# Optimization experiments

Hardware: AMD Instinct MI355X
Metric: run time of the kernel (lower is better)

## Reference

```python
import jax, jax.numpy as jnp
import numpy as np

K = 3
THRESHOLD = 0.05
RADIUS = 0.1
MIN_CORR = 3
MAX_CORR = 1500
N_ITER = 5
EPS = 1e-5
P, N = 1024, 128


def setup_inputs() -> dict:
    key = jax.random.key(0)
    k1, k2, k3, k4, k5 = jax.random.split(key, 5)
    # local knn patches: small spatial extent so matching_radius=0.1 is meaningful
    ref_knn_points = jax.random.normal(k1, (P, N, 3), jnp.float32) * 0.05
    src_knn_points = jax.random.normal(k2, (P, N, 3), jnp.float32) * 0.05
    ref_knn_masks = jax.random.uniform(k3, (P, N)) > 0.1
    src_knn_masks = jax.random.uniform(k4, (P, N)) > 0.1
    matching_score_map = jax.random.normal(k5, (P, N, N), jnp.float32)
    return {
        'ref_knn_points': ref_knn_points,
        'src_knn_points': src_knn_points,
        'ref_knn_masks': ref_knn_masks,
        'src_knn_masks': src_knn_masks,
        'matching_score_map': matching_score_map,
    }


def _kabsch(H, src_c, ref_c, bad):
    # guard degenerate (all-zero-weight) problems with a fixed full-rank H
    safe = jnp.diag(jnp.asarray([3.0, 2.0, 1.0], H.dtype))
    H = jnp.where(bad[..., None, None], safe, H)
    U, S, Vt = jnp.linalg.svd(H)
    V = jnp.swapaxes(Vt, -1, -2)
    Ut = jnp.swapaxes(U, -1, -2)
    det = jnp.linalg.det(V @ Ut)
    D = jnp.zeros_like(H).at[..., 0, 0].set(1.0).at[..., 1, 1].set(1.0).at[..., 2, 2].set(det)
    R = V @ D @ Ut
    t = ref_c - jnp.einsum('...cd,...d->...c', R, src_c)
    T = jnp.zeros(H.shape[:-2] + (4, 4), H.dtype)
    return T.at[..., :3, :3].set(R).at[..., :3, 3].set(t).at[..., 3, 3].set(1.0)


def pair_procrustes(src, ref, w):
    # src, ref: (..., M, 3); w: (..., M)
    tot = jnp.sum(w, -1, keepdims=True)
    wn = w / (tot + EPS)
    src_c = jnp.einsum('...m,...mc->...c', wn, src)
    ref_c = jnp.einsum('...m,...mc->...c', wn, ref)
    H = jnp.einsum('...mc,...m,...md->...cd', src - src_c[..., None, :], wn, ref - ref_c[..., None, :])
    return _kabsch(H, src_c, ref_c, tot[..., 0] < EPS)


def grid_procrustes(src, ref, W):
    # per-proposal weighted Procrustes over the full (ref_i, src_j) pair grid;
    # identical math to gathering nonzero pairs since zero-weight pairs drop out
    tot = jnp.sum(W, (1, 2))  # (P,)
    Wn = W / (tot[:, None, None] + EPS)
    ref_c = jnp.einsum('pij,pic->pc', Wn, ref)
    src_c = jnp.einsum('pij,pjc->pc', Wn, src)
    H = jnp.einsum('pjc,pij,pid->pcd', src - src_c[:, None], Wn, ref - ref_c[:, None])
    return _kabsch(H, src_c, ref_c, tot < EPS)


def _forward(ref_knn_points, src_knn_points, ref_knn_masks, src_knn_masks, matching_score_map):
    Pn, Nn, _ = matching_score_map.shape
    sm = jnp.exp(matching_score_map)
    corr_mask = ref_knn_masks[:, :, None] & src_knn_masks[:, None, :]

    pidx = jnp.arange(Pn)[:, None, None]
    lidx = jnp.arange(Nn)[None, :, None]
    # topk over src dim -> ref_score_map
    ref_ts, ref_ti = jax.lax.top_k(sm, K)
    ref_score_map = jnp.zeros_like(sm).at[pidx, lidx, ref_ti].set(ref_ts)
    # topk over ref dim -> src_score_map (via transpose)
    smT = jnp.swapaxes(sm, 1, 2)
    src_ts, src_ti = jax.lax.top_k(smT, K)
    src_score_map = jnp.swapaxes(jnp.zeros_like(smT).at[pidx, lidx, src_ti].set(src_ts), 1, 2)

    ref_corr = (ref_score_map > THRESHOLD) & corr_mask
    src_corr = (src_score_map > THRESHOLD) & corr_mask
    score_map = 0.5 * (ref_score_map + src_score_map)
    corr_map = ref_corr & src_corr

    # per-proposal Procrustes with pair-grid weights (zero weight = not a corr)
    W = jnp.where(corr_map, score_map, 0.0)
    counts = jnp.sum(corr_map, (1, 2))
    valid = counts >= MIN_CORR
    transforms = grid_procrustes(src_knn_points, ref_knn_points, W)  # (P,4,4)

    # global capped correspondence pool (top MAX_CORR by score)
    flat = jnp.where(corr_map, score_map, -1.0).reshape(-1)
    top_scores, top_flat = jax.lax.top_k(flat, MAX_CORR)
    p = top_flat // (Nn * Nn)
    rem = top_flat % (Nn * Nn)
    i = rem // Nn
    j = rem % Nn
    real = top_scores > 0.0  # padded slots if fewer than MAX_CORR corrs
    corr_scores = jnp.where(real, top_scores, 0.0)
    ref_pts = ref_knn_points[p, i]   # (M,3)
    src_pts = src_knn_points[p, j]   # (M,3)
    # padded candidates pushed far away so they are never inliers
    src_eval = src_pts + jnp.where(real, 0.0, 1e6)[:, None]

    # evaluate every proposal transform on the capped pool, pick max-inlier
    aligned = jnp.einsum('pcd,md->pmc', transforms[:, :3, :3], src_eval) + transforms[:, None, :3, 3]
    d2 = jnp.sum((ref_pts[None] - aligned) ** 2, -1)  # (P,M)
    inliers = d2 < RADIUS ** 2
    icount = jnp.where(valid, jnp.sum(inliers, 1), -1)
    best = jnp.argmax(icount)

    cur = corr_scores * inliers[best].astype(corr_scores.dtype)
    T = pair_procrustes(src_pts, ref_pts, cur)
    for _ in range(N_ITER - 1):
        al = src_eval @ T[:3, :3].T + T[:3, 3]
        d2 = jnp.sum((ref_pts - al) ** 2, -1)
        cur = corr_scores * (d2 < RADIUS ** 2).astype(corr_scores.dtype)
        T = pair_procrustes(src_pts, ref_pts, cur)

    return ref_pts, src_pts, corr_scores, T


def reference(ref_knn_points, src_knn_points, ref_knn_masks, src_knn_masks, matching_score_map):
    return _forward(ref_knn_points, src_knn_points, ref_knn_masks, src_knn_masks, matching_score_map)
```

## Files before the change

kernel.cpp:

```cpp
#include <hip/hip_runtime.h>
#include <math.h>

#define PP    1024
#define NPT   128
#define NN2   16384
#define THRESH 0.05f
#define MAXC  1500
#define EPSD  1e-5
#define RRD   (0.1*0.1)
#define NEGF  -3.0e38f
#define MAXCPB 384
#define SELCAP 4096u

#define OFF_CCNT  0
#define OFF_ICNT  4096
#define OFF_TRANS 8192
#define OFF_POOL  106496
#define OFF_HDR   166496
#define OFF_SEL   166560
#define OFF_PHIST 199328
#define OFF_CLIST 1247904

__device__ inline void top3_upd(float v, float& a, float& b, float& c) {
  float m1 = fminf(a, v);
  a = fmaxf(a, v);
  float m2 = fminf(b, m1);
  b = fmaxf(b, m1);
  c = fmaxf(c, m2);
}
__device__ inline void merge3(float& a, float& b, float& c, float x0, float x1, float x2) {
  float z0 = fmaxf(a, x0);
  float z1 = fmaxf(fminf(a, x0), fmaxf(b, x1));
  float z2 = fmaxf(fmaxf(c, x2), fmaxf(fminf(b, x0), fminf(a, x1)));
  a = z0; b = z1; c = z2;
}

__device__ inline unsigned enc_f(float v) {
  unsigned b = __float_as_uint(v);
  return (b & 0x80000000u) ? ~b : (b | 0x80000000u);
}
__device__ inline float dec_f(unsigned enc) {
  unsigned b = (enc & 0x80000000u) ? (enc ^ 0x80000000u) : ~enc;
  return __uint_as_float(b);
}

__device__ inline void jacobi4(double A[4][4], double V[4][4]) {
  for (int i = 0; i < 4; ++i)
    for (int j = 0; j < 4; ++j) V[i][j] = (i == j) ? 1.0 : 0.0;
  const int PI_[6] = {0, 0, 0, 1, 1, 2};
  const int QI_[6] = {1, 2, 3, 2, 3, 3};
  for (int sweep = 0; sweep < 30; ++sweep) {
    double off = fabs(A[0][1]) + fabs(A[0][2]) + fabs(A[0][3]) +
                 fabs(A[1][2]) + fabs(A[1][3]) + fabs(A[2][3]);
    double dia = fabs(A[0][0]) + fabs(A[1][1]) + fabs(A[2][2]) + fabs(A[3][3]);
    if (off <= 1e-14 * (dia + 1e-300)) break;
    for (int r = 0; r < 6; ++r) {
      int p = PI_[r], q = QI_[r];
      double apq = A[p][q];
      if (fabs(apq) <= 1e-18 * (fabs(A[p][p]) + fabs(A[q][q]) + 1e-300)) continue;
      double theta = (A[q][q] - A[p][p]) / (2.0 * apq);
      double t = ((theta >= 0.0) ? 1.0 : -1.0) / (fabs(theta) + sqrt(1.0 + theta * theta));
      double c = 1.0 / sqrt(1.0 + t * t);
      double s = t * c;
      for (int k = 0; k < 4; ++k) {
        double akp = A[k][p], akq = A[k][q];
        A[k][p] = c * akp - s * akq;
        A[k][q] = s * akp + c * akq;
      }
      for (int k = 0; k < 4; ++k) {
        double apk = A[p][k], aqk = A[q][k];
        A[p][k] = c * apk - s * aqk;
        A[q][k] = s * apk + c * aqk;
      }
      for (int k = 0; k < 4; ++k) {
        double vkp = V[k][p], vkq = V[k][q];
        V[k][p] = c * vkp - s * vkq;
        V[k][q] = s * vkp + c * vkq;
      }
    }
  }
}

__device__ inline double cof3(const double M[4][4], int rr, int cc) {
  int ri[3], ci[3];
  int n = 0;
  for (int i = 0; i < 4; ++i) if (i != rr) ri[n++] = i;
  n = 0;
  for (int j = 0; j < 4; ++j) if (j != cc) ci[n++] = j;
  double a = M[ri[0]][ci[0]], b = M[ri[0]][ci[1]], c = M[ri[0]][ci[2]];
  double d = M[ri[1]][ci[0]], e = M[ri[1]][ci[1]], f = M[ri[1]][ci[2]];
  double g = M[ri[2]][ci[0]], h = M[ri[2]][ci[1]], i2 = M[ri[2]][ci[2]];
  double m = a * (e * i2 - f * h) - b * (d * i2 - f * g) + c * (d * h - e * g);
  return (((rr + cc) & 1) ? -m : m);
}

__device__ inline void kabsch_from_sums(double tot, const double* sr, const double* ss,
                                        const double* m9, double* T12) {
  double den = tot + EPSD;
  double rc[3], sc[3];
  for (int c = 0; c < 3; ++c) { rc[c] = sr[c] / den; sc[c] = ss[c] / den; }
  double sb = tot / den;
  double H[3][3];
  for (int c = 0; c < 3; ++c)
    for (int d = 0; d < 3; ++d)
      H[c][d] = m9[c * 3 + d] / den - (2.0 - sb) * sc[c] * rc[d];
  if (tot < EPSD) {
    H[0][0] = 3.0; H[0][1] = 0.0; H[0][2] = 0.0;
    H[1][0] = 0.0; H[1][1] = 2.0; H[1][2] = 0.0;
    H[2][0] = 0.0; H[2][1] = 0.0; H[2][2] = 1.0;
  }
  double Sxx = H[0][0], Sxy = H[0][1], Sxz = H[0][2];
  double Syx = H[1][0], Syy = H[1][1], Syz = H[1][2];
  double Szx = H[2][0], Szy = H[2][1], Szz = H[2][2];
  double N[4][4] = {
    {Sxx + Syy + Szz, Syz - Szy,        Szx - Sxz,         Sxy - Syx},
    {Syz - Szy,       Sxx - Syy - Szz,  Sxy + Syx,         Szx + Sxz},
    {Szx - Sxz,       Sxy + Syx,       -Sxx + Syy - Szz,   Syz + Szy},
    {Sxy - Syx,       Szx + Sxz,        Syz + Szy,        -Sxx - Syy + Szz}};
  double fro2 = Sxx*Sxx + Sxy*Sxy + Sxz*Sxz + Syx*Syx + Syy*Syy + Syz*Syz +
                Szx*Szx + Szy*Szy + Szz*Szz;
  double c2 = -2.0 * fro2;
  double c1 = -8.0 * (Sxx * (Syy * Szz - Syz * Szy) -
                      Sxy * (Syx * Szz - Syz * Szx) +
                      Sxz * (Syx * Szy - Syy * Szx));
  double c0 = N[0][0] * cof3(N, 0, 0) + N[0][1] * cof3(N, 0, 1) +
              N[0][2] * cof3(N, 0, 2) + N[0][3] * cof3(N, 0, 3);
  double lam = -1e300;
  for (int i = 0; i < 4; ++i) {
    double r = N[i][i];
    for (int j = 0; j < 4; ++j) if (j != i) r += fabs(N[i][j]);
    lam = fmax(lam, r);
  }
  for (int it = 0; it < 100; ++it) {
    double l2 = lam * lam;
    double pv = ((l2 + c2) * lam + c1) * lam + c0;
    double dp = (4.0 * l2 + 2.0 * c2) * lam + c1;
    if (dp == 0.0) break;
    double d = pv / dp;
    lam -= d;
    if (fabs(d) <= 1e-14 * fmax(fabs(lam), 1e-30)) break;
  }
  double K[4][4];
  for (int i = 0; i < 4; ++i)
    for (int j = 0; j < 4; ++j) K[i][j] = N[i][j];
  for (int i = 0; i < 4; ++i) K[i][i] -= lam;
  int jb = 0;
  double bestd = -1.0;
  for (int j = 0; j < 4; ++j) {
    double dj = fabs(cof3(K, j, j));
    if (dj > bestd) { bestd = dj; jb = j; }
  }
  double v[4];
  for (int i = 0; i < 4; ++i) v[i] = cof3(K, jb, i);
  double vn2 = v[0]*v[0] + v[1]*v[1] + v[2]*v[2] + v[3]*v[3];
  double scl = sqrt(fro2) + fabs(lam) + 1e-300;
  double thr = 1e-10 * scl * scl * scl;
  double q0, qx, qy, qz;
  if (vn2 > thr * thr) {
    double inv = 1.0 / sqrt(vn2);
    q0 = v[0] * inv; qx = v[1] * inv; qy = v[2] * inv; qz = v[3] * inv;
  } else {
    double A[4][4], V[4][4];
    for (int i = 0; i < 4; ++i)
      for (int j = 0; j < 4; ++j) A[i][j] = N[i][j];
    jacobi4(A, V);
    int kb = 0; double ev = A[0][0];
    for (int i = 1; i < 4; ++i) if (A[i][i] > ev) { ev = A[i][i]; kb = i; }
    double w0 = V[0][kb], w1 = V[1][kb], w2 = V[2][kb], w3 = V[3][kb];
    double nr = sqrt(w0*w0 + w1*w1 + w2*w2 + w3*w3);
    if (nr < 1e-300) { w0 = 1.0; w1 = w2 = w3 = 0.0; nr = 1.0; }
    q0 = w0 / nr; qx = w1 / nr; qy = w2 / nr; qz = w3 / nr;
  }
  double R[3][3];
  R[0][0] = q0*q0 + qx*qx - qy*qy - qz*qz; R[0][1] = 2.0*(qx*qy - q0*qz); R[0][2] = 2.0*(qx*qz + q0*qy);
  R[1][0] = 2.0*(qx*qy + q0*qz); R[1][1] = q0*q0 - qx*qx + qy*qy - qz*qz; R[1][2] = 2.0*(qy*qz - q0*qx);
  R[2][0] = 2.0*(qx*qz - q0*qy); R[2][1] = 2.0*(qy*qz + q0*qx); R[2][2] = q0*q0 - qx*qx - qy*qy + qz*qz;
  for (int c = 0; c < 3; ++c)
    for (int d = 0; d < 3; ++d) T12[c * 3 + d] = R[c][d];
  for (int c = 0; c < 3; ++c)
    T12[9 + c] = rc[c] - (R[c][0] * sc[0] + R[c][1] * sc[1] + R[c][2] * sc[2]);
}

__global__ __launch_bounds__(256, 2) void k_fused(
    const float* __restrict__ scores, const void* __restrict__ mref,
    const void* __restrict__ msrc, unsigned* __restrict__ ccnt,
    unsigned long long* __restrict__ clist) {
  const int p = blockIdx.x;
  const int tid = threadIdx.x;
  __shared__ float tile[128 * 132];
  __shared__ float colpart[2][NPT][3];
  __shared__ float rthr[NPT], cthr[NPT];
  __shared__ unsigned char lmr[NPT];
  __shared__ unsigned lcnt;
  __shared__ unsigned masku8_s;
  if (tid == 0) lcnt = 0;
  if (tid < 64) {
    unsigned v = (tid < 32) ? ((const unsigned*)mref)[p * 32 + tid]
                            : ((const unsigned*)msrc)[p * 32 + (tid - 32)];
    unsigned long long any = __ballot(v > 1u);
    if (tid == 0) masku8_s = any ? 1u : 0u;
  }
  {
    const float4* S4 = (const float4*)(scores + (size_t)p * NN2);
    float4 vv[16];
#pragma unroll
    for (int s = 0; s < 16; ++s)
      vv[s] = S4[s * 256 + tid];
#pragma unroll
    for (int s = 0; s < 16; ++s) {
      int flat = (s * 256 + tid) * 4;
      int r = flat >> 7, c = flat & 127;
      *(float4*)&tile[r * 132 + c] = vv[s];
    }
  }
  __syncthreads();
  const unsigned maskU8 = masku8_s;
  if (tid < NPT)
    lmr[tid] = maskU8 ? (((const unsigned char*)mref)[p * NPT + tid] != 0)
                      : (((const int*)mref)[p * NPT + tid] != 0);
  const int col = tid & 127;
  const int half = tid >> 7;
  const bool msj = maskU8 ? (((const unsigned char*)msrc)[p * NPT + col] != 0)
                          : (((const int*)msrc)[p * NPT + col] != 0);
  for (int rb = 0; rb < 4; ++rb) {
    int r = rb * 32 + (tid >> 3);
    int o = tid & 7;
    float a = NEGF, b = NEGF, c = NEGF;
    const float4* tr = (const float4*)&tile[r * 132 + o * 16];
#pragma unroll
    for (int k = 0; k < 4; ++k) {
      float4 q = tr[k];
      top3_upd(q.x, a, b, c); top3_upd(q.y, a, b, c);
      top3_upd(q.z, a, b, c); top3_upd(q.w, a, b, c);
    }
#pragma unroll
    for (int m = 1; m < 8; m <<= 1) {
      float pa = __shfl_xor(a, m, 64), pb = __shfl_xor(b, m, 64), pc = __shfl_xor(c, m, 64);
      merge3(a, b, c, pa, pb, pc);
    }
    if (o == 0) rthr[r] = c;
  }
  {
    float a = NEGF, b = NEGF, c = NEGF;
    const float* tc = tile + (half * 64) * 132 + col;
#pragma unroll 8
    for (int r = 0; r < 64; ++r)
      top3_upd(tc[r * 132], a, b, c);
    colpart[half][col][0] = a; colpart[half][col][1] = b; colpart[half][col][2] = c;
  }
  __syncthreads();
  if (tid < NPT) {
    float a = colpart[0][tid][0], b = colpart[0][tid][1], c = colpart[0][tid][2];
    merge3(a, b, c, colpart[1][tid][0], colpart[1][tid][1], colpart[1][tid][2]);
    cthr[tid] = c;
  }
  __syncthreads();
  {
    const float cth = cthr[col];
    const float* tc = tile + (half * 64) * 132 + col;
#pragma unroll 4
    for (int it = 0; it < 64; ++it) {
      float v = tc[it * 132];
      int i = half * 64 + it;
      if (msj && v >= cth && v >= rthr[i] && lmr[i] && (expf(v) > THRESH)) {
        unsigned pos = atomicAdd(&lcnt, 1u);
        if (pos < MAXCPB) {
          unsigned long long key =
              (((unsigned long long)(~enc_f(v))) << 32) |
              (unsigned long long)(unsigned)(p * NN2 + i * NPT + col);
          clist[(size_t)p * MAXCPB + pos] = key;
        }
      }
    }
  }
  __syncthreads();
  if (tid == 0) ccnt[p] = (lcnt < MAXCPB) ? lcnt : MAXCPB;
}

__global__ __launch_bounds__(256) void k_hist(
    const unsigned* __restrict__ ccnt, const unsigned long long* __restrict__ clist,
    unsigned* __restrict__ phist) {
  __shared__ unsigned lh[4096];
  const int b = blockIdx.x, tid = threadIdx.x;
  for (int i = tid; i < 4096; i += 256) lh[i] = 0;
  __syncthreads();
  for (int q = 0; q < 16; ++q) {
    const int p = b * 16 + q;
    const unsigned cnt = min(ccnt[p], (unsigned)MAXCPB);
    const unsigned long long* my = clist + (size_t)p * MAXCPB;
    for (unsigned t = tid; t < cnt; t += 256)
      atomicAdd(&lh[(unsigned)(my[t] >> 52)], 1u);
  }
  __syncthreads();
  for (int i = tid; i < 4096; i += 256) phist[b * 4096 + i] = lh[i];
}

__global__ __launch_bounds__(1024) void k_cut(const unsigned* __restrict__ phist,
                                              unsigned* __restrict__ hdr) {
  __shared__ unsigned s[1024];
  __shared__ unsigned cb_s;
  const int tid = threadIdx.x;
  if (tid == 0) cb_s = 4095u;
  uint4 acc = make_uint4(0, 0, 0, 0);
  const uint4* ph4 = (const uint4*)phist;
#pragma unroll 4
  for (int b = 0; b < 64; ++b) {
    uint4 h = ph4[b * 1024 + tid];
    acc.x += h.x; acc.y += h.y; acc.z += h.z; acc.w += h.w;
  }
  s[tid] = acc.x + acc.y + acc.z + acc.w;
  __syncthreads();
  for (int off = 1; off < 1024; off <<= 1) {
    unsigned v = s[tid];
    unsigned a = (tid >= off) ? s[tid - off] : 0u;
    __syncthreads();
    s[tid] = v + a;
    __syncthreads();
  }
  {
    unsigned pre = (tid > 0) ? s[tid - 1] : 0u;
    unsigned tot4 = acc.x + acc.y + acc.z + acc.w;
    if (pre < MAXC && pre + tot4 >= MAXC) {
      unsigned c0 = pre + acc.x, c1 = c0 + acc.y, c2 = c1 + acc.z;
      cb_s = (c0 >= MAXC) ? tid * 4 : (c1 >= MAXC) ? tid * 4 + 1
           : (c2 >= MAXC) ? tid * 4 + 2 : tid * 4 + 3;
    }
  }
  __syncthreads();
  if (tid == 0) {
    hdr[0] = s[1023];
    hdr[1] = 0u;
    hdr[2] = cb_s;
  }
}

__global__ __launch_bounds__(256) void k_gather(
    const unsigned* __restrict__ ccnt, const unsigned long long* __restrict__ clist,
    unsigned* __restrict__ hdr, unsigned long long* __restrict__ sel) {
  const int b = blockIdx.x, tid = threadIdx.x, lane = tid & 63;
  const unsigned cut = hdr[2];
  for (int q = 0; q < 16; ++q) {
    const int p = b * 16 + q;
    const unsigned cnt = min(ccnt[p], (unsigned)MAXCPB);
    const unsigned long long* my = clist + (size_t)p * MAXCPB;
    for (unsigned t0 = 0; t0 < cnt; t0 += 256) {
      unsigned t = t0 + tid;
      unsigned long long key = 0;
      bool take = false;
      if (t < cnt) {
        key = my[t];
        take = ((unsigned)(key >> 52)) <= cut;
      }
      unsigned long long mb = __ballot(take);
      if (mb) {
        int leader = __ffsll((unsigned long long)mb) - 1;
        unsigned base = 0;
        if (lane == leader) base = atomicAdd(&hdr[1], (unsigned)__popcll(mb));
        base = __shfl(base, leader, 64);
        if (take) {
          unsigned pos = base + (unsigned)__popcll(mb & ((1ull << lane) - 1ull));
          if (pos < SELCAP) sel[pos] = key;
        }
      }
    }
  }
}

__global__ __launch_bounds__(1024) void k_sortout(
    const unsigned long long* __restrict__ sel, const unsigned* __restrict__ hdr,
    const float* __restrict__ refp, const float* __restrict__ srcp,
    float* __restrict__ pool, float* __restrict__ out) {
  __shared__ unsigned long long keys[4096];
  const int tid = threadIdx.x;
  const unsigned sc = min(hdr[1], SELCAP);
  for (unsigned t = tid; t < 4096u; t += 1024)
    keys[t] = (t < sc) ? sel[t] : 0xFFFFFFFFFFFFFFFFull;
  __syncthreads();
  for (unsigned k = 2; k <= 4096; k <<= 1) {
    for (unsigned j = k >> 1; j; j >>= 1) {
      for (unsigned t = tid; t < 4096; t += 1024) {
        unsigned ixj = t ^ j;
        if (ixj > t) {
          unsigned long long A = keys[t], B = keys[ixj];
          bool up = ((t & k) == 0);
          if (up ? (A > B) : (A < B)) { keys[t] = B; keys[ixj] = A; }
        }
      }
      __syncthreads();
    }
  }
  const unsigned stotal = hdr[0];
  const unsigned nreal = (stotal < MAXC) ? stotal : MAXC;
  for (int mm = tid; mm < MAXC; mm += 1024) {
    unsigned flat; float score; bool real = ((unsigned)mm < nreal);
    if (real) {
      unsigned long long key = keys[mm];
      flat = (unsigned)(key & 0xFFFFFFFFull);
      score = expf(dec_f(~(unsigned)(key >> 32)));
    } else {
      flat = (unsigned)mm;
      score = 0.f;
    }
    unsigned p = flat >> 14, rem = flat & 16383u, i = rem >> 7, j = rem & 127u;
    float rx = refp[((size_t)p * NPT + i) * 3 + 0];
    float ry = refp[((size_t)p * NPT + i) * 3 + 1];
    float rz = refp[((size_t)p * NPT + i) * 3 + 2];
    float sx = srcp[((size_t)p * NPT + j) * 3 + 0];
    float sy = srcp[((size_t)p * NPT + j) * 3 + 1];
    float sz = srcp[((size_t)p * NPT + j) * 3 + 2];
    out[mm * 3 + 0] = rx; out[mm * 3 + 1] = ry; out[mm * 3 + 2] = rz;
    out[4500 + mm * 3 + 0] = sx; out[4500 + mm * 3 + 1] = sy; out[4500 + mm * 3 + 2] = sz;
    out[9000 + mm] = score;
    pool[mm * 3 + 0] = rx; pool[mm * 3 + 1] = ry; pool[mm * 3 + 2] = rz;
    pool[4500 + mm * 3 + 0] = sx; pool[4500 + mm * 3 + 1] = sy; pool[4500 + mm * 3 + 2] = sz;
    float pad = real ? 0.f : 1e6f;
    pool[9000 + mm * 3 + 0] = sx + pad;
    pool[9000 + mm * 3 + 1] = sy + pad;
    pool[9000 + mm * 3 + 2] = sz + pad;
    pool[13500 + mm] = score;
  }
}

__global__ __launch_bounds__(256) void k_evalT(
    const unsigned* __restrict__ ccnt, const unsigned long long* __restrict__ clist,
    const float* __restrict__ refp, const float* __restrict__ srcp,
    const float* __restrict__ pool, double* __restrict__ trans,
    int* __restrict__ icount) {
  const int p = blockIdx.x, tid = threadIdx.x, lane = tid & 63;
  __shared__ double red[4][16];
  __shared__ double Ts[12];
  __shared__ int redc[4];
  const unsigned cnt = min(ccnt[p], (unsigned)MAXCPB);
  double tot = 0, sr0 = 0, sr1 = 0, sr2 = 0, ss0 = 0, ss1 = 0, ss2 = 0;
  double m00 = 0, m01 = 0, m02 = 0, m10 = 0, m11 = 0, m12 = 0, m20 = 0, m21 = 0, m22 = 0;
  for (unsigned t = tid; t < cnt; t += 256) {
    unsigned long long key = clist[(size_t)p * MAXCPB + t];
    unsigned flat = (unsigned)(key & 0xFFFFFFFFull);
    unsigned rem = flat & 16383u, i = rem >> 7, j = rem & 127u;
    double w = (double)expf(dec_f(~(unsigned)(key >> 32)));
    double rx = refp[((size_t)p * NPT + i) * 3 + 0];
    double ry = refp[((size_t)p * NPT + i) * 3 + 1];
    double rz = refp[((size_t)p * NPT + i) * 3 + 2];
    double sx = srcp[((size_t)p * NPT + j) * 3 + 0];
    double sy = srcp[((size_t)p * NPT + j) * 3 + 1];
    double sz = srcp[((size_t)p * NPT + j) * 3 + 2];
    tot += w;
    sr0 += w * rx; sr1 += w * ry; sr2 += w * rz;
    ss0 += w * sx; ss1 += w * sy; ss2 += w * sz;
    double wsx = w * sx, wsy = w * sy, wsz = w * sz;
    m00 += wsx * rx; m01 += wsx * ry; m02 += wsx * rz;
    m10 += wsy * rx; m11 += wsy * ry; m12 += wsy * rz;
    m20 += wsz * rx; m21 += wsz * ry; m22 += wsz * rz;
  }
  double vals[16] = {tot, sr0, sr1, sr2, ss0, ss1, ss2,
                     m00, m01, m02, m10, m11, m12, m20, m21, m22};
#pragma unroll
  for (int k = 0; k < 16; ++k) {
    double x = vals[k];
    for (int o = 32; o; o >>= 1) x += __shfl_down(x, o, 64);
    if (lane == 0) red[tid >> 6][k] = x;
  }
  __syncthreads();
  if (tid == 0) {
    double s16[16];
    for (int k = 0; k < 16; ++k)
      s16[k] = red[0][k] + red[1][k] + red[2][k] + red[3][k];
    kabsch_from_sums(s16[0], s16 + 1, s16 + 4, s16 + 7, Ts);
    for (int k = 0; k < 12; ++k) trans[p * 12 + k] = Ts[k];
  }
  __syncthreads();
  double R00 = Ts[0], R01 = Ts[1], R02 = Ts[2], R10 = Ts[3], R11 = Ts[4], R12 = Ts[5];
  double R20 = Ts[6], R21 = Ts[7], R22 = Ts[8], t0 = Ts[9], t1 = Ts[10], t2 = Ts[11];
  const float* pr = pool;
  const float* pe = pool + 9000;
  int c = 0;
  for (int mm = tid; mm < MAXC; mm += 256) {
    double ex = pe[mm * 3], ey = pe[mm * 3 + 1], ez = pe[mm * 3 + 2];
    double ax = R00 * ex + R01 * ey + R02 * ez + t0;
    double ay = R10 * ex + R11 * ey + R12 * ez + t1;
    double az = R20 * ex + R21 * ey + R22 * ez + t2;
    double dx = pr[mm * 3] - ax, dy = pr[mm * 3 + 1] - ay, dz = pr[mm * 3 + 2] - az;
    if (dx * dx + dy * dy + dz * dz < RRD) ++c;
  }
  for (int o = 32; o; o >>= 1) c += __shfl_down(c, o, 64);
  if (lane == 0) redc[tid >> 6] = c;
  __syncthreads();
  if (tid == 0) {
    int tc = redc[0] + redc[1] + redc[2] + redc[3];
    icount[p] = (cnt >= 3u) ? tc : -1;
  }
}

__global__ __launch_bounds__(256, 1) void k_refine(const double* __restrict__ trans,
                                                   const int* __restrict__ icount,
                                                   const float* __restrict__ pool,
                                                   float* __restrict__ out) {
  const int tid = threadIdx.x, lane = tid & 63;
  __shared__ int rc_[256], ri_[256];
  __shared__ double red[4][16];
  __shared__ double T[12];
  int bc = -2147483647, bi = 0;
  for (int idx = tid; idx < PP; idx += 256) {
    int c = icount[idx];
    if (c > bc) { bc = c; bi = idx; }
  }
  rc_[tid] = bc; ri_[tid] = bi;
  __syncthreads();
  for (int s = 128; s; s >>= 1) {
    if (tid < s) {
      int c2 = rc_[tid + s], i2 = ri_[tid + s];
      if (c2 > rc_[tid] || (c2 == rc_[tid] && i2 < ri_[tid])) { rc_[tid] = c2; ri_[tid] = i2; }
    }
    __syncthreads();
  }
  if (tid == 0) {
    int best = ri_[0];
    for (int k = 0; k < 12; ++k) T[k] = trans[best * 12 + k];
  }
  __syncthreads();
  const float* pr = pool;
  const float* ps = pool + 4500;
  const float* pe = pool + 9000;
  const float* pw = pool + 13500;
  for (int iter = 0; iter < 5; ++iter) {
    double R00 = T[0], R01 = T[1], R02 = T[2], R10 = T[3], R11 = T[4], R12 = T[5];
    double R20 = T[6], R21 = T[7], R22 = T[8], t0 = T[9], t1 = T[10], t2 = T[11];
    double tot = 0, sr0 = 0, sr1 = 0, sr2 = 0, ss0 = 0, ss1 = 0, ss2 = 0;
    double m00 = 0, m01 = 0, m02 = 0, m10 = 0, m11 = 0, m12 = 0, m20 = 0, m21 = 0, m22 = 0;
    for (int mm = tid; mm < MAXC; mm += 256) {
      double ex = pe[mm * 3], ey = pe[mm * 3 + 1], ez = pe[mm * 3 + 2];
      double ax = R00 * ex + R01 * ey + R02 * ez + t0;
      double ay = R10 * ex + R11 * ey + R12 * ez + t1;
      double az = R20 * ex + R21 * ey + R22 * ez + t2;
      double rx = pr[mm * 3], ry = pr[mm * 3 + 1], rz = pr[mm * 3 + 2];
      double dx = rx - ax, dy = ry - ay, dz = rz - az;
      if (dx * dx + dy * dy + dz * dz < RRD) {
        double w = (double)pw[mm];
        double sx = ps[mm * 3], sy = ps[mm * 3 + 1], sz = ps[mm * 3 + 2];
        tot += w;
        sr0 += w * rx; sr1 += w * ry; sr2 += w * rz;
        ss0 += w * sx; ss1 += w * sy; ss2 += w * sz;
        double wsx = w * sx, wsy = w * sy, wsz = w * sz;
        m00 += wsx * rx; m01 += wsx * ry; m02 += wsx * rz;
        m10 += wsy * rx; m11 += wsy * ry; m12 += wsy * rz;
        m20 += wsz * rx; m21 += wsz * ry; m22 += wsz * rz;
      }
    }
    double vals[16] = {tot, sr0, sr1, sr2, ss0, ss1, ss2,
                       m00, m01, m02, m10, m11, m12, m20, m21, m22};
#pragma unroll
    for (int k = 0; k < 16; ++k) {
      double x = vals[k];
      for (int o = 32; o; o >>= 1) x += __shfl_down(x, o, 64);
      if (lane == 0) red[tid >> 6][k] = x;
    }
    __syncthreads();
    if (tid == 0) {
      double s16[16];
      for (int k = 0; k < 16; ++k)
        s16[k] = red[0][k] + red[1][k] + red[2][k] + red[3][k];
      kabsch_from_sums(s16[0], s16 + 1, s16 + 4, s16 + 7, T);
    }
    __syncthreads();
  }
  if (tid == 0) {
    out[10500 + 0]  = (float)T[0]; out[10500 + 1]  = (float)T[1];
    out[10500 + 2]  = (float)T[2]; out[10500 + 3]  = (float)T[9];
    out[10500 + 4]  = (float)T[3]; out[10500 + 5]  = (float)T[4];
    out[10500 + 6]  = (float)T[5]; out[10500 + 7]  = (float)T[10];
    out[10500 + 8]  = (float)T[6]; out[10500 + 9]  = (float)T[7];
    out[10500 + 10] = (float)T[8]; out[10500 + 11] = (float)T[11];
    out[10500 + 12] = 0.f; out[10500 + 13] = 0.f;
    out[10500 + 14] = 0.f; out[10500 + 15] = 1.f;
  }
}

extern "C" void kernel_launch(void* const* d_in, const int* in_sizes, int n_in,
                              void* d_out, int out_size, void* d_ws, size_t ws_size,
                              hipStream_t stream) {
  const float* refp = (const float*)d_in[0];
  const float* srcp = (const float*)d_in[1];
  const void* mref = d_in[2];
  const void* msrc = d_in[3];
  const float* scores = (const float*)d_in[4];
  float* out = (float*)d_out;
  char* ws = (char*)d_ws;
  unsigned* ccnt = (unsigned*)(ws + OFF_CCNT);
  int* icount = (int*)(ws + OFF_ICNT);
  double* trans = (double*)(ws + OFF_TRANS);
  float* pool = (float*)(ws + OFF_POOL);
  unsigned* hdr = (unsigned*)(ws + OFF_HDR);
  unsigned long long* sel = (unsigned long long*)(ws + OFF_SEL);
  unsigned* phist = (unsigned*)(ws + OFF_PHIST);
  unsigned long long* clist = (unsigned long long*)(ws + OFF_CLIST);

  k_fused<<<PP, 256, 0, stream>>>(scores, mref, msrc, ccnt, clist);
  k_hist<<<64, 256, 0, stream>>>(ccnt, clist, phist);
  k_cut<<<1, 1024, 0, stream>>>(phist, hdr);
  k_gather<<<64, 256, 0, stream>>>(ccnt, clist, hdr, sel);
  k_sortout<<<1, 1024, 0, stream>>>(sel, hdr, refp, srcp, pool, out);
  k_evalT<<<PP, 256, 0, stream>>>(ccnt, clist, refp, srcp, pool, trans, icount);
  k_refine<<<1, 256, 0, stream>>>(trans, icount, pool, out);
}
```

Baseline: 325.2 us.

## Restructure bitonic sort with wave-local stages and adaptive sort size

The single-block bitonic sort now sorts only 2048 keys when the selected count fits, which cuts the number of stages. Each compare-exchange is indexed by pair, so no thread sits idle on a failed ixj>t check. Once the stride drops below a per-wave chunk, each wavefront finishes the small-stride stages on its own slice with no block-wide __syncthreads. Correctness now relies on lockstep execution within a wavefront and on LDS accesses staying ordered without an explicit barrier or fence.

After: 296.8 us. 1.1x faster.

```diff
diff --git a/kernel.cpp b/kernel.cpp
--- a/kernel.cpp
+++ b/kernel.cpp
@@ -373,21 +373,36 @@
   __shared__ unsigned long long keys[4096];
   const int tid = threadIdx.x;
   const unsigned sc = min(hdr[1], SELCAP);
-  for (unsigned t = tid; t < 4096u; t += 1024)
+  const unsigned n2 = (sc <= 2048u) ? 2048u : 4096u;
+  for (unsigned t = tid; t < n2; t += 1024)
     keys[t] = (t < sc) ? sel[t] : 0xFFFFFFFFFFFFFFFFull;
   __syncthreads();
-  for (unsigned k = 2; k <= 4096; k <<= 1) {
-    for (unsigned j = k >> 1; j; j >>= 1) {
-      for (unsigned t = tid; t < 4096; t += 1024) {
-        unsigned ixj = t ^ j;
-        if (ixj > t) {
-          unsigned long long A = keys[t], B = keys[ixj];
-          bool up = ((t & k) == 0);
-          if (up ? (A > B) : (A < B)) { keys[t] = B; keys[ixj] = A; }
-        }
+  const unsigned chunk = n2 >> 4;
+  const unsigned w = tid >> 6, lane = tid & 63;
+  const unsigned base = w * chunk;
+  for (unsigned k = 2; k <= n2; k <<= 1) {
+    unsigned j = k >> 1;
+    for (; j >= chunk; j >>= 1) {
+      for (unsigned q = tid; q < (n2 >> 1); q += 1024) {
+        unsigned t = ((q & ~(j - 1u)) << 1) | (q & (j - 1u));
+        unsigned u = t | j;
+        bool up = ((t & k) == 0u);
+        unsigned long long A = keys[t], B = keys[u];
+        if (up ? (A > B) : (A < B)) { keys[t] = B; keys[u] = A; }
       }
       __syncthreads();
     }
+    for (; j; j >>= 1) {
+      for (unsigned q = lane; q < (chunk >> 1); q += 64) {
+        unsigned lt = ((q & ~(j - 1u)) << 1) | (q & (j - 1u));
+        unsigned t = base + lt;
+        unsigned u = t | j;
+        bool up = ((t & k) == 0u);
+        unsigned long long A = keys[t], B = keys[u];
+        if (up ? (A > B) : (A < B)) { keys[t] = B; keys[u] = A; }
+      }
+    }
+    __syncthreads();
   }
   const unsigned stotal = hdr[0];
   const unsigned nreal = (stotal < MAXC) ? stotal : MAXC;
```
